# Kernel tuning notes

Hardware: AMD Instinct MI355X
Metric: run time of the kernel (lower is better)

## Reference

```python
import jax, jax.numpy as jnp
import numpy as np

CTX_WIN = 3  # config.ctx_win_size


def setup_inputs() -> dict:
    key = jax.random.key(0)
    k1, k2, k3 = jax.random.split(key, 3)
    bsz, seq_len, h1, A = 32, 2048, 128, 8
    batch_docIn = jax.random.normal(k1, (bsz, seq_len, h1), dtype=jnp.float32)
    mask = jnp.ones((bsz, seq_len), dtype=bool)
    # params initialized uniform(-0.01, 0.01) as in the torch module
    aspEmbed_weight = jax.random.uniform(k2, (A, CTX_WIN * h1), minval=-0.01, maxval=0.01, dtype=jnp.float32)
    aspProj = jax.random.uniform(k3, (A, h1, h1), minval=-0.01, maxval=0.01, dtype=jnp.float32)
    return {"batch_docIn": batch_docIn, "mask": mask,
            "aspEmbed_weight": aspEmbed_weight, "aspProj": aspProj}


def reference(batch_docIn, mask, aspEmbed_weight, aspProj):
    b, s, h = batch_docIn.shape
    A = aspProj.shape[0]
    win = CTX_WIN
    pad = (win - 1) // 2

    # all aspects at once: [b, A, s, h]
    proj = jnp.einsum('bsd,adh->bash', batch_docIn, aspProj)
    padded = jnp.pad(proj, ((0, 0), (0, 0), (pad, pad), (0, 0)))

    embedR = aspEmbed_weight.reshape(A, h, win)
    # scores[b,a,s] = sum_{d,w} window[b,a,s,d,w] * embedR[a,d,w]
    # computed as a sum over the (small, fixed) window offsets to avoid
    scores = sum(jnp.einsum('bash,ah->bas', padded[:, :, w:w + s, :], embedR[:, :, w])
                 for w in range(win))

    # mask (bool [b,s]) -> masked_fill(~mask, -inf); softmax over seq dim
    scores = jnp.where(mask[:, None, :], scores, -jnp.inf)
    attn = jax.nn.softmax(scores, axis=-1)  # [b, A, s]

    # weighted sum over sequence: [b, A, h]
    rep = jnp.einsum('bash,bas->bah', proj, attn)

    # torch returns attn as [b, A, s] (after transpose/cat) and rep [b, A, h]
    return attn, rep
```

## Files before the change

### kernel.cpp

```cpp
#include <hip/hip_runtime.h>
#include <math.h>

#define BB 32
#define SS 2048
#define HH 128
#define AA 8

typedef _Float16 h2 __attribute__((ext_vector_type(2)));
typedef _Float16 h8 __attribute__((ext_vector_type(8)));
typedef _Float16 f16x8 __attribute__((ext_vector_type(8)));
typedef float f32x4 __attribute__((ext_vector_type(4)));


__global__ __launch_bounds__(128) void prep_kernel(const float* __restrict__ embed,
                                                   const float* __restrict__ proj,
                                                   uint4* __restrict__ bfrag) {
    __shared__ float ua[HH][3];
    int a = blockIdx.x;
    int d = threadIdx.x;
    const float* P = proj + ((size_t)a * HH + d) * HH;
    const float* E = embed + a * (3 * HH);
    float a0 = 0.f, a1 = 0.f, a2 = 0.f;
    for (int h = 0; h < HH; ++h) {
        float x = P[h];
        a0 += x * E[h * 3 + 0];
        a1 += x * E[h * 3 + 1];
        a2 += x * E[h * 3 + 2];
    }
    ua[d][0] = a0; ua[d][1] = a1; ua[d][2] = a2;
    __syncthreads();

    for (int i = d; i < 96; i += 128) {
        int kk = i >> 3, e = i & 7;
        f16x8 v = {0, 0, 0, 0, 0, 0, 0, 0};
        int lane;
        if (e < 4) {
            int q = e;
            lane = q * 16 + a;
            #pragma unroll
            for (int j = 0; j < 8; ++j) {
                int k = kk * 32 + q * 8 + j;
                int w = k >> 7, dd = k & 127;
                v[j] = (_Float16)ua[dd][w];
            }
        } else {
            lane = (e - 4) * 16 + a + 8;
        }
        bfrag[kk * 64 + lane] = __builtin_bit_cast(uint4, v);
    }
}

__global__ __launch_bounds__(256, 4) void tile_kernel(const float* __restrict__ doc,
                                                      const int* __restrict__ mask,
                                                      const uint4* __restrict__ bfrag,
                                                      float* __restrict__ E,
                                                      float* __restrict__ Zpart,
                                                      float* __restrict__ pools) {
    __shared__ __align__(16) unsigned char smraw[21312];
    h2*    dt    = (h2*)smraw;
    float* etile = (float*)(smraw + 19008);
    float* zred  = (float*)(smraw + 19008 + 2048);

    int t = threadIdx.x;
    int lane = t & 63, wave = t >> 6;
    int tile = blockIdx.x;
    int b = blockIdx.y;
    int s0 = tile * 64;

    for (int idx = t; idx < 66 * 16; idx += 256) {
        int row = idx >> 4, c = idx & 15;
        int srow = s0 - 1 + row;
        h8 hv = {0, 0, 0, 0, 0, 0, 0, 0};
        if (srow >= 0 && srow < SS) {
            const float4* src = (const float4*)(doc + ((size_t)b * SS + srow) * HH + c * 8);
            float4 v0 = src[0], v1 = src[1];
            hv[0] = (_Float16)v0.x; hv[1] = (_Float16)v0.y;
            hv[2] = (_Float16)v0.z; hv[3] = (_Float16)v0.w;
            hv[4] = (_Float16)v1.x; hv[5] = (_Float16)v1.y;
            hv[6] = (_Float16)v1.z; hv[7] = (_Float16)v1.w;
        }
        *(h8*)(dt + row * 72 + c * 4) = hv;
    }

    f16x8 bf[12];
    #pragma unroll
    for (int kk = 0; kk < 12; ++kk)
        bf[kk] = __builtin_bit_cast(f16x8, bfrag[kk * 64 + lane]);
    __syncthreads();

    f32x4 acc = {0.f, 0.f, 0.f, 0.f};
    #pragma unroll
    for (int kk = 0; kk < 12; ++kk) {
        int w = kk >> 2;
        int row = wave * 16 + (lane & 15) + w;
        int colh2 = (kk & 3) * 16 + (lane >> 4) * 4;
        f16x8 af = *(const f16x8*)(dt + row * 72 + colh2);
        acc = __builtin_amdgcn_mfma_f32_16x16x32_f16(af, bf[kk], acc, 0, 0, 0);
    }

    const int* mrow = mask + (size_t)b * SS + s0;
    {
        int a = lane & 15;
        int rbase = wave * 16 + (lane >> 4) * 4;
        if (a < 8) {
            #pragma unroll
            for (int jj = 0; jj < 4; ++jj) {
                int sl2 = rbase + jj;
                float e = mrow[sl2] ? __expf(acc[jj]) : 0.f;
                E[((size_t)(b * AA + a)) * SS + s0 + sl2] = e;
                etile[sl2 * 8 + a] = e;
            }
        }
    }
    __syncthreads();
    if (t < 64) {
        int a = t & 7, g = t >> 3;
        float p = 0.f;
        #pragma unroll
        for (int k = 0; k < 8; ++k) p += etile[(g * 8 + k) * 8 + a];
        zred[g * 8 + a] = p;
    }
    __syncthreads();
    if (t < 8) {
        float z = 0.f;
        #pragma unroll
        for (int g = 0; g < 8; ++g) z += zred[g * 8 + t];
        Zpart[((size_t)(b * AA + t)) * 32 + tile] = z;
    }

    int dq = t & 31, sub = t >> 5;
    float4 pacc[8];
    #pragma unroll
    for (int a = 0; a < 8; ++a) pacc[a] = make_float4(0.f, 0.f, 0.f, 0.f);
    for (int i = 0; i < 8; ++i) {
        int row = 1 + sub * 8 + i;
        uint2 X = *(const uint2*)(dt + row * 72 + dq * 2);
        h2 lo = __builtin_bit_cast(h2, X.x), hi = __builtin_bit_cast(h2, X.y);
        float x0 = (float)lo[0], x1 = (float)lo[1];
        float x2 = (float)hi[0], x3 = (float)hi[1];
        #pragma unroll
        for (int a = 0; a < 8; ++a) {
            float w = etile[(sub * 8 + i) * 8 + a];
            pacc[a].x += w * x0; pacc[a].y += w * x1;
            pacc[a].z += w * x2; pacc[a].w += w * x3;
        }
    }
    #pragma unroll
    for (int a = 0; a < 8; ++a) {
        pacc[a].x += __shfl_xor(pacc[a].x, 32);
        pacc[a].y += __shfl_xor(pacc[a].y, 32);
        pacc[a].z += __shfl_xor(pacc[a].z, 32);
        pacc[a].w += __shfl_xor(pacc[a].w, 32);
    }
    __syncthreads();
    float* cs2 = (float*)smraw;
    if ((t & 63) < 32) {
        #pragma unroll
        for (int a = 0; a < 8; ++a)
            *(float4*)(cs2 + (wave * 8 + a) * 128 + dq * 4) = pacc[a];
    }
    __syncthreads();
    for (int oi = t; oi < 1024; oi += 256) {
        int a = oi >> 7, d = oi & 127;
        float v = (cs2[(0 * 8 + a) * 128 + d] + cs2[(1 * 8 + a) * 128 + d]) +
                  (cs2[(2 * 8 + a) * 128 + d] + cs2[(3 * 8 + a) * 128 + d]);
        pools[(((size_t)(b * 32 + tile)) * AA + a) * HH + d] = v;
    }
}

__global__ __launch_bounds__(256) void finalize_kernel(const float* __restrict__ E,
                                                       const float* __restrict__ Zpart,
                                                       const float* __restrict__ pools,
                                                       const float* __restrict__ proj,
                                                       float* __restrict__ attn,
                                                       float* __restrict__ rep) {
    __shared__ float zbuf[256];
    __shared__ float invZ[8];
    __shared__ float ctxp[2][128];
    __shared__ float ctx[128];
    __shared__ float seg[8][32];
    int t = threadIdx.x;
    int ck = blockIdx.x;
    int b = blockIdx.y;
    int a_rep = ck & 7, hq = ck >> 3;

    zbuf[t] = Zpart[((size_t)(b * AA + (t >> 5))) * 32 + (t & 31)];
    __syncthreads();
    if (t < 8) {
        float z = 0.f;
        #pragma unroll
        for (int k = 0; k < 32; ++k) z += zbuf[t * 32 + k];
        invZ[t] = 1.0f / z;
    }
    __syncthreads();

    for (int oi = t; oi < 512; oi += 256) {
        int a = oi >> 6, s = oi & 63;
        size_t idx = ((size_t)(b * AA + a)) * SS + ck * 64 + s;
        attn[idx] = E[idx] * invZ[a];
    }

    {
        int d = t & 127, half = t >> 7;
        float v = 0.f;
        for (int c = half * 16; c < half * 16 + 16; ++c)
            v += pools[(((size_t)(b * 32 + c)) * AA + a_rep) * HH + d];
        ctxp[half][d] = v;
    }
    __syncthreads();
    if (t < 128) ctx[t] = (ctxp[0][t] + ctxp[1][t]) * invZ[a_rep];
    __syncthreads();

    {
        int h = hq * 32 + (t & 31), sg = t >> 5;
        float v = 0.f;
        for (int d = sg * 16; d < sg * 16 + 16; ++d)
            v += ctx[d] * proj[((size_t)a_rep * HH + d) * HH + h];
        seg[sg][t & 31] = v;
    }
    __syncthreads();
    if (t < 32) {
        float v = 0.f;
        #pragma unroll
        for (int sg = 0; sg < 8; ++sg) v += seg[sg][t];
        rep[((size_t)(b * AA + a_rep)) * HH + hq * 32 + t] = v;
    }
}

extern "C" void kernel_launch(void* const* d_in, const int* in_sizes, int n_in,
                              void* d_out, int out_size, void* d_ws, size_t ws_size,
                              hipStream_t stream) {
    const float* doc   = (const float*)d_in[0];
    const int*   mask  = (const int*)d_in[1];
    const float* embed = (const float*)d_in[2];
    const float* proj  = (const float*)d_in[3];

    float* out  = (float*)d_out;
    float* attn = out;
    float* rep  = out + (size_t)BB * AA * SS;

    uint4* bfrag = (uint4*)d_ws;
    float* E     = (float*)d_ws + 4096;
    float* Zp    = E + (size_t)BB * AA * SS;
    float* pools = Zp + (size_t)BB * AA * 32;

    prep_kernel<<<8, 128, 0, stream>>>(embed, proj, bfrag);
    tile_kernel<<<dim3(32, 32), 256, 0, stream>>>(doc, mask, bfrag, E, Zp, pools);
    finalize_kernel<<<dim3(32, 32), 256, 0, stream>>>(E, Zp, pools, proj, attn, rep);
}
```

Before: 28.35 us.

## Parallelize prep kernel, vectorize E stores, split finalize into attn and rep blocks

The prep kernel now runs 32 blocks instead of 8, each staging a 32-row slice of the projection and the embedding in shared memory before computing its part of the fused score weights. The tile kernel writes its exp scores as one float4 per lane instead of four scalar stores. Finalize becomes a 1D grid where 1024 blocks only normalize attn with float4 accesses and 256 blocks each compute one (b,a) rep row. Before, every finalize block redundantly re-reduced the pools for its aspect, so the rep work was repeated four times. The aim is to cut the serial prep latency and the redundant finalize work, at the cost of more launch-shape complexity.

```diff
diff --git a/kernel.cpp b/kernel.cpp
--- a/kernel.cpp
+++ b/kernel.cpp
@@ -15,34 +15,37 @@
 __global__ __launch_bounds__(128) void prep_kernel(const float* __restrict__ embed,
                                                    const float* __restrict__ proj,
                                                    uint4* __restrict__ bfrag) {
-    __shared__ float ua[HH][3];
-    int a = blockIdx.x;
-    int d = threadIdx.x;
-    const float* P = proj + ((size_t)a * HH + d) * HH;
-    const float* E = embed + a * (3 * HH);
-    float a0 = 0.f, a1 = 0.f, a2 = 0.f;
-    for (int h = 0; h < HH; ++h) {
-        float x = P[h];
-        a0 += x * E[h * 3 + 0];
-        a1 += x * E[h * 3 + 1];
-        a2 += x * E[h * 3 + 2];
-    }
-    ua[d][0] = a0; ua[d][1] = a1; ua[d][2] = a2;
-    __syncthreads();
-
-    for (int i = d; i < 96; i += 128) {
-        int kk = i >> 3, e = i & 7;
+    __shared__ float pl[32][129];
+    __shared__ float eb[384];
+    __shared__ float ub[32][3];
+    int t = threadIdx.x;
+    int a = blockIdx.x >> 2, dc = blockIdx.x & 3;
+
+    for (int i = t; i < 32 * 128; i += 128) {
+        int r = i >> 7, h = i & 127;
+        pl[r][h] = proj[((size_t)a * HH + dc * 32 + r) * HH + h];
+    }
+    for (int i = t; i < 384; i += 128) eb[i] = embed[a * 384 + i];
+    __syncthreads();
+
+    if (t < 96) {
+        int w = t / 32, dl = t % 32;
+        float acc = 0.f;
+        for (int h = 0; h < HH; ++h) acc += pl[dl][h] * eb[h * 3 + w];
+        ub[dl][w] = acc;
+    }
+    __syncthreads();
+
+    if (t < 24) {
+        int kk = dc + (t >> 3) * 4, e = t & 7;
         f16x8 v = {0, 0, 0, 0, 0, 0, 0, 0};
         int lane;
         if (e < 4) {
             int q = e;
             lane = q * 16 + a;
+            int w = kk >> 2;
             #pragma unroll
-            for (int j = 0; j < 8; ++j) {
-                int k = kk * 32 + q * 8 + j;
-                int w = k >> 7, dd = k & 127;
-                v[j] = (_Float16)ua[dd][w];
-            }
+            for (int j = 0; j < 8; ++j) v[j] = (_Float16)ub[q * 8 + j][w];
         } else {
             lane = (e - 4) * 16 + a + 8;
         }
@@ -103,13 +106,16 @@
         int a = lane & 15;
         int rbase = wave * 16 + (lane >> 4) * 4;
         if (a < 8) {
+            float4 ev;
+            float* evp = (float*)&ev;
             #pragma unroll
             for (int jj = 0; jj < 4; ++jj) {
                 int sl2 = rbase + jj;
                 float e = mrow[sl2] ? __expf(acc[jj]) : 0.f;
-                E[((size_t)(b * AA + a)) * SS + s0 + sl2] = e;
+                evp[jj] = e;
                 etile[sl2 * 8 + a] = e;
             }
+            *(float4*)(E + ((size_t)(b * AA + a)) * SS + s0 + rbase) = ev;
         }
     }
     __syncthreads();
@@ -174,56 +180,66 @@
                                                        const float* __restrict__ proj,
                                                        float* __restrict__ attn,
                                                        float* __restrict__ rep) {
-    __shared__ float zbuf[256];
-    __shared__ float invZ[8];
-    __shared__ float ctxp[2][128];
-    __shared__ float ctx[128];
-    __shared__ float seg[8][32];
     int t = threadIdx.x;
-    int ck = blockIdx.x;
-    int b = blockIdx.y;
-    int a_rep = ck & 7, hq = ck >> 3;
-
-    zbuf[t] = Zpart[((size_t)(b * AA + (t >> 5))) * 32 + (t & 31)];
-    __syncthreads();
-    if (t < 8) {
-        float z = 0.f;
-        #pragma unroll
-        for (int k = 0; k < 32; ++k) z += zbuf[t * 32 + k];
-        invZ[t] = 1.0f / z;
-    }
-    __syncthreads();
-
-    for (int oi = t; oi < 512; oi += 256) {
-        int a = oi >> 6, s = oi & 63;
-        size_t idx = ((size_t)(b * AA + a)) * SS + ck * 64 + s;
-        attn[idx] = E[idx] * invZ[a];
+    int id = blockIdx.x;
+
+    if (id < 1024) {
+        __shared__ float zbuf[256];
+        __shared__ float invZ[8];
+        int b = id >> 5, ck = id & 31;
+        zbuf[t] = Zpart[((size_t)(b * AA + (t >> 5))) * 32 + (t & 31)];
+        __syncthreads();
+        if (t < 8) {
+            float z = 0.f;
+            #pragma unroll
+            for (int k = 0; k < 32; ++k) z += zbuf[t * 32 + k];
+            invZ[t] = 1.0f / z;
+        }
+        __syncthreads();
+        if (t < 128) {
+            int a = t >> 4, s4 = (t & 15) * 4;
+            size_t idx = ((size_t)(b * AA + a)) * SS + ck * 64 + s4;
+            float4 ev = *(const float4*)(E + idx);
+            float iz = invZ[a];
+            ev.x *= iz; ev.y *= iz; ev.z *= iz; ev.w *= iz;
+            *(float4*)(attn + idx) = ev;
+        }
+        return;
     }
 
     {
-        int d = t & 127, half = t >> 7;
-        float v = 0.f;
-        for (int c = half * 16; c < half * 16 + 16; ++c)
-            v += pools[(((size_t)(b * 32 + c)) * AA + a_rep) * HH + d];
-        ctxp[half][d] = v;
-    }
-    __syncthreads();
-    if (t < 128) ctx[t] = (ctxp[0][t] + ctxp[1][t]) * invZ[a_rep];
-    __syncthreads();
-
-    {
-        int h = hq * 32 + (t & 31), sg = t >> 5;
-        float v = 0.f;
-        for (int d = sg * 16; d < sg * 16 + 16; ++d)
-            v += ctx[d] * proj[((size_t)a_rep * HH + d) * HH + h];
-        seg[sg][t & 31] = v;
-    }
-    __syncthreads();
-    if (t < 32) {
-        float v = 0.f;
-        #pragma unroll
-        for (int sg = 0; sg < 8; ++sg) v += seg[sg][t];
-        rep[((size_t)(b * AA + a_rep)) * HH + hq * 32 + t] = v;
+        __shared__ float invz;
+        __shared__ float ctxp[2][128];
+        __shared__ float ctx[128];
+        __shared__ float hred[2][128];
+        int r = id - 1024;
+        int b = r >> 3, a = r & 7;
+        if (t == 0) {
+            float z = 0.f;
+            for (int k = 0; k < 32; ++k)
+                z += Zpart[((size_t)(b * AA + a)) * 32 + k];
+            invz = 1.0f / z;
+        }
+        {
+            int d = t & 127, half = t >> 7;
+            float v = 0.f;
+            for (int c = half * 16; c < half * 16 + 16; ++c)
+                v += pools[(((size_t)(b * 32 + c)) * AA + a) * HH + d];
+            ctxp[half][d] = v;
+        }
+        __syncthreads();
+        if (t < 128) ctx[t] = (ctxp[0][t] + ctxp[1][t]) * invz;
+        __syncthreads();
+        {
+            int h = t & 127, dh = t >> 7;
+            float v = 0.f;
+            for (int d = dh * 64; d < dh * 64 + 64; ++d)
+                v += ctx[d] * proj[((size_t)a * HH + d) * HH + h];
+            hred[dh][h] = v;
+        }
+        __syncthreads();
+        if (t < 128)
+            rep[((size_t)(b * AA + a)) * HH + t] = hred[0][t] + hred[1][t];
     }
 }
 
@@ -244,7 +260,7 @@
     float* Zp    = E + (size_t)BB * AA * SS;
     float* pools = Zp + (size_t)BB * AA * 32;
 
-    prep_kernel<<<8, 128, 0, stream>>>(embed, proj, bfrag);
+    prep_kernel<<<32, 128, 0, stream>>>(embed, proj, bfrag);
     tile_kernel<<<dim3(32, 32), 256, 0, stream>>>(doc, mask, bfrag, E, Zp, pools);
-    finalize_kernel<<<dim3(32, 32), 256, 0, stream>>>(E, Zp, pools, proj, attn, rep);
-}
+    finalize_kernel<<<1280, 256, 0, stream>>>(E, Zp, pools, proj, attn, rep);
+}
```

Measured after the change: 36.93 us. 1.3x slower.
